# Kernel optimization log

Measured on AMD Instinct MI355X. Metric: run time of the kernel, lower is better.

## Reference

```python
import jax, jax.numpy as jnp
import numpy as np

B, S, D_IN, D_OUT = 4, 2048, 1024, 1024

def setup_inputs() -> dict:
    key = jax.random.key(0)
    ks = jax.random.split(key, 6)
    s = 1.0 / np.sqrt(D_IN)
    return {
        "inputs": jax.random.normal(ks[0], (B, S, D_IN), dtype=jnp.float32),
        "Wq": jax.random.normal(ks[1], (D_IN, D_OUT), dtype=jnp.float32) * s,
        "Wk": jax.random.normal(ks[2], (D_IN, D_OUT), dtype=jnp.float32) * s,
        "Wv": jax.random.normal(ks[3], (D_IN, D_OUT), dtype=jnp.float32) * s,
        "Wo": jax.random.normal(ks[4], (D_OUT, D_OUT), dtype=jnp.float32) * (1.0 / np.sqrt(D_OUT)),
        "bo": jax.random.normal(ks[5], (D_OUT,), dtype=jnp.float32) * 0.01,
    }

def reference(inputs, Wq, Wk, Wv, Wo, bo):
    # QKV projections (no bias, matching qkv_bias=False)
    q = inputs @ Wq  # [B,S,D]
    k = inputs @ Wk
    v = inputs @ Wv
    # naive full attention: scores [B,S,S]
    scores = jnp.einsum('bqd,bkd->bqk', q, k) / jnp.sqrt(jnp.asarray(k.shape[-1], q.dtype))
    attn = jax.nn.softmax(scores, axis=-1)
    out = jnp.einsum('bqk,bkd->bqd', attn, v)
    return out @ Wo + bo
```

## Files before the change

kernel.cpp:

```cpp
#include <hip/hip_runtime.h>
#include <hip/hip_bf16.h>
#include <cstdint>

typedef __attribute__((ext_vector_type(8))) __bf16 bf16x8;
typedef __attribute__((ext_vector_type(4))) float  f32x4;

__device__ __forceinline__ unsigned short f2bf(float x) {
    union { float f; unsigned u; } v; v.f = x;
    unsigned r = v.u + 0x7fffu + ((v.u >> 16) & 1u);
    return (unsigned short)(r >> 16);
}
__device__ __forceinline__ unsigned pack2bf(float a, float b) {
    return (unsigned)f2bf(a) | ((unsigned)f2bf(b) << 16);
}

__device__ __forceinline__ void gld_lds16(const unsigned short* g, unsigned short* l) {
    __builtin_amdgcn_global_load_lds(
        (const __attribute__((address_space(1))) unsigned int*)g,
        (__attribute__((address_space(3))) unsigned int*)l,
        16, 0, 0);
}

__global__ void cvt_kernel(const float* __restrict__ in, unsigned short* __restrict__ out, int n4) {
    int i = blockIdx.x * blockDim.x + threadIdx.x;
    if (i < n4) {
        float4 f = ((const float4*)in)[i];
        ushort4 o;
        o.x = f2bf(f.x); o.y = f2bf(f.y); o.z = f2bf(f.z); o.w = f2bf(f.w);
        ((ushort4*)out)[i] = o;
    }
}

__global__ void zero_kernel(float* __restrict__ p, int n) {
    int i = blockIdx.x * blockDim.x + threadIdx.x;
    if (i < n) p[i] = 0.f;
}

__global__ void wpack_kernel(const float* __restrict__ W, unsigned short* __restrict__ out) {
    int tid  = threadIdx.x;
    int lane = tid & 63;
    int chunk = blockIdx.x * 4 + (tid >> 6);
    int nt = chunk >> 5, k32 = chunk & 31;
    int r = lane & 15, q = lane >> 4;
    const float* src = W + (size_t)(k32*32 + q*8) * 1024 + nt*16 + r;
    unsigned o[4];
#pragma unroll
    for (int i = 0; i < 4; i++)
        o[i] = pack2bf(src[(size_t)(2*i) * 1024], src[(size_t)(2*i+1) * 1024]);
    *(uint4*)(out + (size_t)chunk * 512 + lane * 8) = make_uint4(o[0], o[1], o[2], o[3]);
}

template<int EPI>
__global__ __launch_bounds__(512, 2)
void gemm8p(const unsigned short* __restrict__ A, const unsigned short* __restrict__ Bpk,
            void* __restrict__ C, unsigned short* __restrict__ Ck, unsigned short* __restrict__ Cv,
            int lda, int ldc, int KS, int ns, float scale,
            long long sA, long long sB, long long sC)
{
    __shared__ __align__(16) char smem[131072];

    const int tid  = threadIdx.x;
    const int lane = tid & 63;
    const int wave = tid >> 6;
    const int bz = blockIdx.z;
    A   += (size_t)bz * sA;
    Bpk += (size_t)bz * sB;

    const int gx = gridDim.x;
    int lin = blockIdx.y * gx + blockIdx.x;
    int cpx = (gx * gridDim.y) >> 3;
    int swz = (lin & 7) * cpx + (lin >> 3);
    const int bm = (swz / gx) * 256;
    const int bn = (swz % gx) * 256;

    const int wm = (wave & 1) * 128;
    const int wn = (wave >> 1) * 64;
    const int ln15 = lane & 15;
    const int quad = lane >> 4;
    const int fko = (quad ^ ((ln15 >> 1) & 3)) * 8;

    const int srow = tid >> 2;
    const int scol = ((tid & 3) ^ ((tid >> 3) & 3)) * 8;
    const unsigned short* paU = A + (size_t)(bm + srow) * lda + scol;
    const unsigned short* paL = A + (size_t)(bm + 128 + srow) * lda + scol;
    const unsigned short* pb0 = Bpk + (size_t)((bn >> 4) + (tid >> 6)) * KS * 512 + lane * 8;
    const long long pbstep = (long long)8 * KS * 512;

    f32x4 acc[8][4];
#pragma unroll
    for (int i = 0; i < 8; i++)
#pragma unroll
        for (int j = 0; j < 4; j++) acc[i][j] = (f32x4){0.f, 0.f, 0.f, 0.f};

    auto stageA = [&](int buf, int t, int k) {
        char* d = smem + buf * 32768 + k * 16384 + tid * 16;
        const unsigned short* s = paU + t * 64 + k * 32;
        gld_lds16(s, (unsigned short*)d);
        gld_lds16(paL + t * 64 + k * 32, (unsigned short*)(d + 8192));
    };
    auto stageB = [&](int buf, int t, int k) {
        char* d = smem + 65536 + buf * 32768 + k * 16384 + (tid >> 6) * 1024 + lane * 16;
        const unsigned short* s = pb0 + (size_t)(2 * t + k) * 512;
        gld_lds16(s, (unsigned short*)d);
        gld_lds16(s + pbstep, (unsigned short*)(d + 8192));
    };
    auto dsread12 = [&](int buf, int k, bf16x8* af, bf16x8* bfr) {
        const unsigned short* Ar = (const unsigned short*)(smem + buf * 32768 + k * 16384);
        const unsigned short* Br = (const unsigned short*)(smem + 65536 + buf * 32768 + k * 16384);
#pragma unroll
        for (int im = 0; im < 8; im++)
            af[im] = *(const bf16x8*)&Ar[(wm + (im >> 2) * 64 + (im & 3) * 16 + ln15) * 32 + fko];
#pragma unroll
        for (int j = 0; j < 4; j++)
            bfr[j] = *(const bf16x8*)&Br[((wn >> 4) + j) * 512 + lane * 8];
    };
    auto mfma32 = [&](const bf16x8* af, const bf16x8* bfr) {
        __builtin_amdgcn_s_setprio(1);
#pragma unroll
        for (int im = 0; im < 8; im++)
#pragma unroll
            for (int j = 0; j < 4; j++)
                acc[im][j] = __builtin_amdgcn_mfma_f32_16x16x32_bf16(
                    af[im], bfr[j], acc[im][j], 0, 0, 0);
        __builtin_amdgcn_s_setprio(0);
    };

#define BAR   __builtin_amdgcn_s_barrier()
#define FEN   asm volatile("" ::: "memory")
#define VM4   asm volatile("s_waitcnt vmcnt(4)" ::: "memory")

    stageB(0, 0, 0); stageA(0, 0, 0); stageB(0, 0, 1); stageA(0, 0, 1);
    VM4; BAR; FEN;

    bf16x8 af[8], bfr[4];
    for (int t = 0; t < ns; ++t) {
        const int buf = t & 1, nb = buf ^ 1;
        const int tn = (t + 1 < ns) ? t + 1 : 0;
        dsread12(buf, 0, af, bfr);
        stageB(nb, tn, 0); stageA(nb, tn, 0);
        mfma32(af, bfr);
        VM4;
        BAR; FEN;
        dsread12(buf, 1, af, bfr);
        stageB(nb, tn, 1); stageA(nb, tn, 1);
        mfma32(af, bfr);
        VM4;
        BAR; FEN;
    }
#undef BAR
#undef FEN
#undef VM4

    if (EPI == 1 || EPI == 3) {
        __syncthreads();
        float* ep = (float*)(smem + wave * 4352);
        unsigned short* Co = (unsigned short*)C + (size_t)bz * sC;
        float* rsb = (EPI == 3) ? ((float*)Ck + (size_t)bz * 2048) : nullptr;
#pragma unroll
        for (int im = 0; im < 8; im++) {
            int mrow = (im >> 2) * 64 + (im & 3) * 16;
            if (EPI == 3) {
                float ev[4][4];
                float psum[4] = {0.f, 0.f, 0.f, 0.f};
#pragma unroll
                for (int j = 0; j < 4; j++)
#pragma unroll
                    for (int r = 0; r < 4; r++) {
                        ev[j][r] = __expf(acc[im][j][r] * scale);
                        psum[r] += ev[j][r];
                        ep[(quad*4 + r) * 68 + j*16 + ln15] = ev[j][r];
                    }
#pragma unroll
                for (int r = 0; r < 4; r++) {
                    float v = psum[r];
                    v += __shfl_xor(v, 1, 64);
                    v += __shfl_xor(v, 2, 64);
                    v += __shfl_xor(v, 4, 64);
                    v += __shfl_xor(v, 8, 64);
                    if (ln15 == 0)
                        atomicAdd(&rsb[bm + wm + mrow + quad*4 + r], v);
                }
            } else {
#pragma unroll
                for (int j = 0; j < 4; j++)
#pragma unroll
                    for (int r = 0; r < 4; r++)
                        ep[(quad*4 + r) * 68 + j*16 + ln15] = acc[im][j][r] * scale;
            }
            __builtin_amdgcn_s_waitcnt(0);
#pragma unroll
            for (int pp = 0; pp < 2; pp++) {
                int lrow = pp*8 + (lane >> 3);
                int col0 = (lane & 7) * 8;
                float4 lo = *(const float4*)&ep[lrow * 68 + col0];
                float4 hi = *(const float4*)&ep[lrow * 68 + col0 + 4];
                uint4 o;
                o.x = pack2bf(lo.x, lo.y); o.y = pack2bf(lo.z, lo.w);
                o.z = pack2bf(hi.x, hi.y); o.w = pack2bf(hi.z, hi.w);
                *(uint4*)&Co[(size_t)(bm + wm + mrow + lrow) * ldc + bn + wn + col0] = o;
            }
            __builtin_amdgcn_s_waitcnt(0);
        }
    } else {
        __syncthreads();
        float* ep = (float*)(smem + wave * 8704);
        const int region = bn >> 10;
#pragma unroll
        for (int g = 0; g < 4; g++) {
#pragma unroll
            for (int ii = 0; ii < 2; ii++) {
                int im = g*2 + ii;
#pragma unroll
                for (int j = 0; j < 4; j++)
#pragma unroll
                    for (int r = 0; r < 4; r++)
                        ep[(ii*16 + quad*4 + r) * 68 + j*16 + ln15] = acc[im][j][r] * scale;
            }
            __builtin_amdgcn_s_waitcnt(0);
            const int mrow0 = bm + wm + g*32;
            if (region == 0) {
                unsigned short* Q = (unsigned short*)C;
#pragma unroll
                for (int pp = 0; pp < 4; pp++) {
                    int lrow = pp*8 + (lane >> 3);
                    int col0 = (lane & 7) * 8;
                    float4 lo = *(const float4*)&ep[lrow * 68 + col0];
                    float4 hi = *(const float4*)&ep[lrow * 68 + col0 + 4];
                    uint4 o;
                    o.x = pack2bf(lo.x, lo.y); o.y = pack2bf(lo.z, lo.w);
                    o.z = pack2bf(hi.x, hi.y); o.w = pack2bf(hi.z, hi.w);
                    *(uint4*)&Q[(size_t)(mrow0 + lrow) * ldc + bn + wn + col0] = o;
                }
            } else {
#pragma unroll
                for (int mt = 0; mt < 2; mt++)
#pragma unroll
                    for (int c = 0; c < 2; c++) {
                        float4 f0 = *(const float4*)&ep[(mt*16 + ln15) * 68 + c*32 + quad*8];
                        float4 f1 = *(const float4*)&ep[(mt*16 + ln15) * 68 + c*32 + quad*8 + 4];
                        uint4 o;
                        o.x = pack2bf(f0.x, f0.y); o.y = pack2bf(f0.z, f0.w);
                        o.z = pack2bf(f1.x, f1.y); o.w = pack2bf(f1.z, f1.w);
                        int cid = ((mrow0 + mt*16) >> 4) * 32 + ((bn - 1024 + wn + c*32) >> 5);
                        *(uint4*)(Ck + (size_t)cid * 512 + lane * 8) = o;
                    }
            }
            __builtin_amdgcn_s_waitcnt(0);
        }
    }
}

template<int EPI>
__global__ __launch_bounds__(512, 2)
void gemm_pk(const unsigned short* __restrict__ A, const unsigned short* __restrict__ Bpk,
             void* __restrict__ C, unsigned short* __restrict__ Ck, unsigned short* __restrict__ Cv,
             const float* __restrict__ bias,
             int lda, int ldc, int KS, int ns, float scale,
             long long sA, long long sB, long long sC)
{
    __shared__ __align__(16) char smem[98304];

    const int tid  = threadIdx.x;
    const int lane = tid & 63;
    const int wave = tid >> 6;
    const int bz = blockIdx.z;
    A   += (size_t)bz * sA;
    Bpk += (size_t)bz * sB;

    const int gx = gridDim.x;
    int lin = blockIdx.y * gx + blockIdx.x;
    int cpx = (gx * gridDim.y) >> 3;
    int swz = (lin & 7) * cpx + (lin >> 3);
    const int bm = (swz / gx) * 256;
    const int bn = (swz % gx) * 128;

    const int srow = tid >> 2;
    const int scol = ((tid & 3) ^ ((tid >> 3) & 3)) * 8;
    const unsigned short* pa0 = A + (size_t)(bm + srow) * lda + scol;
    const unsigned short* pa1 = pa0 + 32;
    const unsigned short* pa2 = A + (size_t)(bm + 128 + srow) * lda + scol;
    const unsigned short* pa3 = pa2 + 32;

    const int wm = (wave & 3) * 64;
    const int wn = (wave >> 2) * 64;
    const int ln15 = lane & 15;
    const int quad = lane >> 4;
    const int fko = (quad ^ ((ln15 >> 1) & 3)) * 8;
    const int rbase = (wm >> 7) * 4096 + (wm & 127) * 32;
    const int ldsoff = tid * 16;

    const unsigned short* pb[4];
#pragma unroll
    for (int j = 0; j < 4; j++)
        pb[j] = Bpk + (size_t)(((bn + wn + j*16) >> 4) * KS) * 512 + lane * 8;

    f32x4 acc[4][4];
#pragma unroll
    for (int i = 0; i < 4; i++)
#pragma unroll
        for (int j = 0; j < 4; j++) acc[i][j] = (f32x4){0.f, 0.f, 0.f, 0.f};

    auto dma = [&](int buf) {
        char* base = smem + buf * 32768;
        gld_lds16(pa0, (unsigned short*)(base + ldsoff));
        gld_lds16(pa2, (unsigned short*)(base + 8192  + ldsoff));
        gld_lds16(pa1, (unsigned short*)(base + 16384 + ldsoff));
        gld_lds16(pa3, (unsigned short*)(base + 24576 + ldsoff));
        pa0 += 64; pa1 += 64; pa2 += 64; pa3 += 64;
    };
    auto loadB = [&](bf16x8* br) {
#pragma unroll
        for (int j = 0; j < 4; j++) {
            br[j]     = *(const bf16x8*)(pb[j]);
            br[4 + j] = *(const bf16x8*)(pb[j] + 512);
            pb[j] += 1024;
        }
    };
    auto phase = [&](const unsigned short* As, int t, const bf16x8* br) {
        bf16x8 af[4];
#pragma unroll
        for (int i = 0; i < 4; i++)
            af[i] = *(const bf16x8*)&As[t*8192 + rbase + i*512 + ln15*32 + fko];
        __builtin_amdgcn_s_setprio(1);
#pragma unroll
        for (int i = 0; i < 4; i++)
#pragma unroll
            for (int j = 0; j < 4; j++)
                acc[i][j] = __builtin_amdgcn_mfma_f32_16x16x32_bf16(
                    af[i], br[t*4 + j], acc[i][j], 0, 0, 0);
        __builtin_amdgcn_s_setprio(0);
    };

#define SB __builtin_amdgcn_sched_barrier(0)
    bf16x8 b0[8], b1[8];
    SB; dma(0); SB; loadB(b0); SB; dma(1); SB;

    int p = 0;
    for (int it = 0; it < ns; it += 2) {
        const unsigned short* As0 = (const unsigned short*)(smem + p * 32768);
        int p1 = p + 1; if (p1 >= 3) p1 -= 3;
        int q0 = p + 2; if (q0 >= 3) q0 -= 3;
        const unsigned short* As1 = (const unsigned short*)(smem + p1 * 32768);
        const bool more = (it + 2 < ns);

        asm volatile("s_waitcnt vmcnt(12)" ::: "memory");
        SB; __builtin_amdgcn_s_barrier(); SB;
        loadB(b1); SB;
        phase(As0, 0, b0);
        __builtin_amdgcn_s_barrier(); SB;
        if (more) { dma(q0); SB; }
        phase(As0, 1, b0);

        if (more) { asm volatile("s_waitcnt vmcnt(12)" ::: "memory"); }
        else      { asm volatile("s_waitcnt vmcnt(8)"  ::: "memory"); }
        SB; __builtin_amdgcn_s_barrier(); SB;
        if (more) { loadB(b0); SB; }
        phase(As1, 0, b1);
        __builtin_amdgcn_s_barrier(); SB;
        if (it + 3 < ns) { dma(p); SB; }
        phase(As1, 1, b1);

        p = q0;
    }
#undef SB

    if (EPI == 0) {
        float bval[4];
#pragma unroll
        for (int j = 0; j < 4; j++) bval[j] = bias[bn + wn + j*16 + ln15];
        float* Co = (float*)C + (size_t)bz * sC;
#pragma unroll
        for (int i = 0; i < 4; i++) {
            int r0 = bm + wm + i*16 + quad*4;
#pragma unroll
            for (int j = 0; j < 4; j++) {
                int c = bn + wn + j*16 + ln15;
#pragma unroll
                for (int r = 0; r < 4; r++)
                    Co[(size_t)(r0 + r) * ldc + c] = acc[i][j][r] * scale + bval[j];
            }
        }
    } else if (EPI == 1) {
        __syncthreads();
        float* ep = (float*)(smem + wave * 4352);
        unsigned short* Co = (unsigned short*)C + (size_t)bz * sC;
        const float* rsb = bias ? bias + (size_t)bz * 2048 : nullptr;
#pragma unroll
        for (int i = 0; i < 4; i++) {
            float sc[4];
#pragma unroll
            for (int r = 0; r < 4; r++)
                sc[r] = rsb ? (1.0f / rsb[bm + wm + i*16 + quad*4 + r]) : scale;
#pragma unroll
            for (int j = 0; j < 4; j++)
#pragma unroll
                for (int r = 0; r < 4; r++)
                    ep[(quad*4 + r) * 68 + j*16 + ln15] = acc[i][j][r] * sc[r];
            __builtin_amdgcn_s_waitcnt(0);
#pragma unroll
            for (int pp = 0; pp < 2; pp++) {
                int lrow = pp*8 + (lane >> 3);
                int col0 = (lane & 7) * 8;
                float4 lo = *(const float4*)&ep[lrow * 68 + col0];
                float4 hi = *(const float4*)&ep[lrow * 68 + col0 + 4];
                uint4 o;
                o.x = pack2bf(lo.x, lo.y); o.y = pack2bf(lo.z, lo.w);
                o.z = pack2bf(hi.x, hi.y); o.w = pack2bf(hi.z, hi.w);
                *(uint4*)&Co[(size_t)(bm + wm + i*16 + lrow) * ldc + bn + wn + col0] = o;
            }
            __builtin_amdgcn_s_waitcnt(0);
        }
    } else {
        __syncthreads();
        float* ep = (float*)(smem + wave * 8704);
#pragma unroll
        for (int g = 0; g < 2; g++) {
#pragma unroll
            for (int ii = 0; ii < 2; ii++) {
                int i = g*2 + ii;
#pragma unroll
                for (int j = 0; j < 4; j++)
#pragma unroll
                    for (int r = 0; r < 4; r++)
                        ep[(ii*16 + quad*4 + r) * 68 + j*16 + ln15] = acc[i][j][r];
            }
            __builtin_amdgcn_s_waitcnt(0);
            const int mrow0 = bm + wm + g*32;
            const int s32 = mrow0 >> 5;
#pragma unroll
            for (int dt = 0; dt < 4; dt++) {
                float v[8];
#pragma unroll
                for (int e = 0; e < 8; e++)
                    v[e] = ep[(quad*8 + e) * 68 + dt*16 + ln15];
                uint4 o;
                o.x = pack2bf(v[0], v[1]); o.y = pack2bf(v[2], v[3]);
                o.z = pack2bf(v[4], v[5]); o.w = pack2bf(v[6], v[7]);
                int cid = (((bn + wn) >> 4) + dt) * 256 + s32;
                *(uint4*)(Cv + (size_t)cid * 512 + lane * 8) = o;
            }
            __builtin_amdgcn_s_waitcnt(0);
        }
    }
}

extern "C" void kernel_launch(void* const* d_in, const int* in_sizes, int n_in,
                              void* d_out, int out_size, void* d_ws, size_t ws_size,
                              hipStream_t stream) {
    const float* X  = (const float*)d_in[0];
    const float* Wq = (const float*)d_in[1];
    const float* Wk = (const float*)d_in[2];
    const float* Wv = (const float*)d_in[3];
    const float* Wo = (const float*)d_in[4];
    const float* bo = (const float*)d_in[5];
    float* out = (float*)d_out;

    size_t off = 0;
    auto alloc = [&](size_t bytes) {
        void* p = (char*)d_ws + off;
        off += (bytes + 255) & ~(size_t)255;
        return p;
    };
    unsigned short* Xbf  = (unsigned short*)alloc(8192ull * 1024 * 2);
    unsigned short* Wpk  = (unsigned short*)alloc(192ull * 32 * 512 * 2);
    unsigned short* Wopk = (unsigned short*)alloc(64ull * 32 * 512 * 2);
    unsigned short* Qrm  = (unsigned short*)alloc(8192ull * 1024 * 2);
    unsigned short* Kpk  = (unsigned short*)alloc(512ull * 32 * 512 * 2);
    unsigned short* Vpk  = (unsigned short*)alloc(64ull * 256 * 512 * 2);
    unsigned short* Sc   = (unsigned short*)alloc(4ull * 2048 * 2048 * 2);
    float*          RS   = (float*)alloc(4ull * 2048 * 4);
    unsigned short* AO   = Xbf;

    cvt_kernel<<<(8192*1024/4 + 255)/256, 256, 0, stream>>>(X, Xbf, 8192*1024/4);
    zero_kernel<<<(8192 + 255)/256, 256, 0, stream>>>(RS, 4*2048);
    wpack_kernel<<<512, 256, 0, stream>>>(Wq, Wpk);
    wpack_kernel<<<512, 256, 0, stream>>>(Wk, Wpk + 64*32*512);
    wpack_kernel<<<512, 256, 0, stream>>>(Wv, Wpk + 128*32*512);
    wpack_kernel<<<512, 256, 0, stream>>>(Wo, Wopk);

    gemm8p<2><<<dim3(2048/256, 8192/256, 1), 512, 0, stream>>>(
        Xbf, Wpk, Qrm, Kpk, nullptr, 1024, 1024, 32, 16, 1.0f, 0, 0, 0);

    gemm_pk<4><<<dim3(1024/128, 8192/256, 1), 512, 0, stream>>>(
        Xbf, Wpk + 128*32*512, nullptr, nullptr, Vpk, nullptr,
        1024, 0, 32, 16, 1.0f, 0, 0, 0);

    gemm8p<3><<<dim3(2048/256, 2048/256, 4), 512, 0, stream>>>(
        Qrm, Kpk, Sc, (unsigned short*)RS, nullptr, 1024, 2048, 32, 16, 0.03125f,
        2048ll*1024, 128ll*32*512, 2048ll*2048);

    gemm_pk<1><<<dim3(1024/128, 2048/256, 4), 512, 0, stream>>>(
        Sc, Vpk, AO, nullptr, nullptr, RS, 2048, 1024, 256, 32, 1.0f,
        2048ll*2048, 64ll*512, 2048ll*1024);

    gemm_pk<0><<<dim3(1024/128, 8192/256, 1), 512, 0, stream>>>(
        AO, Wopk, out, nullptr, nullptr, bo, 1024, 1024, 32, 16, 1.0f, 0, 0, 0);

    (void)n_in; (void)in_sizes; (void)out_size; (void)ws_size;
}
```

Baseline: 282.0 us.

## Fuse Q/K/V projections into one GEMM and merge prep kernels

Extends the gemm8p QK projection grid to 3072 output columns so the V projection is computed in the same launch, with a third epilogue region writing the packed V layout. The separate gemm_pk V launch is dropped. The zero kernel is folded into the fp32-to-bf16 conversion kernel, and the four weight-pack launches become one. This cuts launch count and tail effects and runs all projections on the larger 256x256 tile kernel, at the cost of a third branch in the epilogue.

```diff
diff --git a/kernel.cpp b/kernel.cpp
--- a/kernel.cpp
+++ b/kernel.cpp
@@ -21,8 +21,10 @@
         16, 0, 0);
 }
 
-__global__ void cvt_kernel(const float* __restrict__ in, unsigned short* __restrict__ out, int n4) {
+__global__ void cvt_kernel(const float* __restrict__ in, unsigned short* __restrict__ out,
+                           int n4, float* __restrict__ rs) {
     int i = blockIdx.x * blockDim.x + threadIdx.x;
+    if (i < 8192) rs[i] = 0.f;
     if (i < n4) {
         float4 f = ((const float4*)in)[i];
         ushort4 o;
@@ -31,15 +33,18 @@
     }
 }
 
-__global__ void zero_kernel(float* __restrict__ p, int n) {
-    int i = blockIdx.x * blockDim.x + threadIdx.x;
-    if (i < n) p[i] = 0.f;
-}
-
-__global__ void wpack_kernel(const float* __restrict__ W, unsigned short* __restrict__ out) {
+__global__ void wpack4_kernel(const float* __restrict__ Wq, const float* __restrict__ Wk,
+                              const float* __restrict__ Wv, const float* __restrict__ Wo,
+                              unsigned short* __restrict__ Wpk, unsigned short* __restrict__ Wopk) {
+    int m = blockIdx.x >> 9;
+    const float* W = (m == 0) ? Wq : (m == 1) ? Wk : (m == 2) ? Wv : Wo;
+    unsigned short* out = (m == 0) ? Wpk
+                        : (m == 1) ? Wpk + 64*32*512
+                        : (m == 2) ? Wpk + 128*32*512
+                        : Wopk;
     int tid  = threadIdx.x;
     int lane = tid & 63;
-    int chunk = blockIdx.x * 4 + (tid >> 6);
+    int chunk = (blockIdx.x & 511) * 4 + (tid >> 6);
     int nt = chunk >> 5, k32 = chunk & 31;
     int r = lane & 15, q = lane >> 4;
     const float* src = W + (size_t)(k32*32 + q*8) * 1024 + nt*16 + r;
@@ -231,7 +236,7 @@
                     o.z = pack2bf(hi.x, hi.y); o.w = pack2bf(hi.z, hi.w);
                     *(uint4*)&Q[(size_t)(mrow0 + lrow) * ldc + bn + wn + col0] = o;
                 }
-            } else {
+            } else if (region == 1) {
 #pragma unroll
                 for (int mt = 0; mt < 2; mt++)
 #pragma unroll
@@ -244,6 +249,20 @@
                         int cid = ((mrow0 + mt*16) >> 4) * 32 + ((bn - 1024 + wn + c*32) >> 5);
                         *(uint4*)(Ck + (size_t)cid * 512 + lane * 8) = o;
                     }
+            } else {
+                int s32 = mrow0 >> 5;
+#pragma unroll
+                for (int dt = 0; dt < 4; dt++) {
+                    float v[8];
+#pragma unroll
+                    for (int e = 0; e < 8; e++)
+                        v[e] = ep[(quad*8 + e) * 68 + dt*16 + ln15];
+                    uint4 o;
+                    o.x = pack2bf(v[0], v[1]); o.y = pack2bf(v[2], v[3]);
+                    o.z = pack2bf(v[4], v[5]); o.w = pack2bf(v[6], v[7]);
+                    int cid = (((bn - 2048 + wn) >> 4) + dt) * 256 + s32;
+                    *(uint4*)(Cv + (size_t)cid * 512 + lane * 8) = o;
+                }
             }
             __builtin_amdgcn_s_waitcnt(0);
         }
@@ -380,7 +399,7 @@
                     Co[(size_t)(r0 + r) * ldc + c] = acc[i][j][r] * scale + bval[j];
             }
         }
-    } else if (EPI == 1) {
+    } else {
         __syncthreads();
         float* ep = (float*)(smem + wave * 4352);
         unsigned short* Co = (unsigned short*)C + (size_t)bz * sC;
@@ -407,37 +426,6 @@
                 o.x = pack2bf(lo.x, lo.y); o.y = pack2bf(lo.z, lo.w);
                 o.z = pack2bf(hi.x, hi.y); o.w = pack2bf(hi.z, hi.w);
                 *(uint4*)&Co[(size_t)(bm + wm + i*16 + lrow) * ldc + bn + wn + col0] = o;
-            }
-            __builtin_amdgcn_s_waitcnt(0);
-        }
-    } else {
-        __syncthreads();
-        float* ep = (float*)(smem + wave * 8704);
-#pragma unroll
-        for (int g = 0; g < 2; g++) {
-#pragma unroll
-            for (int ii = 0; ii < 2; ii++) {
-                int i = g*2 + ii;
-#pragma unroll
-                for (int j = 0; j < 4; j++)
-#pragma unroll
-                    for (int r = 0; r < 4; r++)
-                        ep[(ii*16 + quad*4 + r) * 68 + j*16 + ln15] = acc[i][j][r];
-            }
-            __builtin_amdgcn_s_waitcnt(0);
-            const int mrow0 = bm + wm + g*32;
-            const int s32 = mrow0 >> 5;
-#pragma unroll
-            for (int dt = 0; dt < 4; dt++) {
-                float v[8];
-#pragma unroll
-                for (int e = 0; e < 8; e++)
-                    v[e] = ep[(quad*8 + e) * 68 + dt*16 + ln15];
-                uint4 o;
-                o.x = pack2bf(v[0], v[1]); o.y = pack2bf(v[2], v[3]);
-                o.z = pack2bf(v[4], v[5]); o.w = pack2bf(v[6], v[7]);
-                int cid = (((bn + wn) >> 4) + dt) * 256 + s32;
-                *(uint4*)(Cv + (size_t)cid * 512 + lane * 8) = o;
             }
             __builtin_amdgcn_s_waitcnt(0);
         }
@@ -471,19 +459,11 @@
     float*          RS   = (float*)alloc(4ull * 2048 * 4);
     unsigned short* AO   = Xbf;
 
-    cvt_kernel<<<(8192*1024/4 + 255)/256, 256, 0, stream>>>(X, Xbf, 8192*1024/4);
-    zero_kernel<<<(8192 + 255)/256, 256, 0, stream>>>(RS, 4*2048);
-    wpack_kernel<<<512, 256, 0, stream>>>(Wq, Wpk);
-    wpack_kernel<<<512, 256, 0, stream>>>(Wk, Wpk + 64*32*512);
-    wpack_kernel<<<512, 256, 0, stream>>>(Wv, Wpk + 128*32*512);
-    wpack_kernel<<<512, 256, 0, stream>>>(Wo, Wopk);
-
-    gemm8p<2><<<dim3(2048/256, 8192/256, 1), 512, 0, stream>>>(
-        Xbf, Wpk, Qrm, Kpk, nullptr, 1024, 1024, 32, 16, 1.0f, 0, 0, 0);
-
-    gemm_pk<4><<<dim3(1024/128, 8192/256, 1), 512, 0, stream>>>(
-        Xbf, Wpk + 128*32*512, nullptr, nullptr, Vpk, nullptr,
-        1024, 0, 32, 16, 1.0f, 0, 0, 0);
+    cvt_kernel<<<(8192*1024/4 + 255)/256, 256, 0, stream>>>(X, Xbf, 8192*1024/4, RS);
+    wpack4_kernel<<<2048, 256, 0, stream>>>(Wq, Wk, Wv, Wo, Wpk, Wopk);
+
+    gemm8p<2><<<dim3(3072/256, 8192/256, 1), 512, 0, stream>>>(
+        Xbf, Wpk, Qrm, Kpk, Vpk, 1024, 1024, 32, 16, 1.0f, 0, 0, 0);
 
     gemm8p<3><<<dim3(2048/256, 2048/256, 4), 512, 0, stream>>>(
         Qrm, Kpk, Sc, (unsigned short*)RS, nullptr, 1024, 2048, 32, 16, 0.03125f,
```

Result: no change. 278.4 us (median of 2 runs) (-1.3%).
